# Optimization experiments

Hardware: AMD Instinct MI355X
Metric: run time of the kernel (lower is better)

Reference implementation:

```python
import jax, jax.numpy as jnp
import numpy as np

V, E, HID, T = 50000, 256, 512, 12   # vocab, embed dim, lstm hidden (bi total), tagset size
START, STOP = 10, 11
L = 2048                              # sentence length
H = HID // 2                          # per-direction hidden
NEG = -10000.0


def setup_inputs():
    key = jax.random.key(0)
    ks = jax.random.split(key, 13)
    s = 0.05
    sentence = jax.random.randint(ks[0], (L,), 0, V)
    embed = jax.random.normal(ks[1], (V, E), jnp.float32) * s
    w_ih_f = jax.random.normal(ks[2], (4 * H, E), jnp.float32) * s
    w_hh_f = jax.random.normal(ks[3], (4 * H, H), jnp.float32) * s
    b_ih_f = jax.random.normal(ks[4], (4 * H,), jnp.float32) * s
    b_hh_f = jax.random.normal(ks[5], (4 * H,), jnp.float32) * s
    w_ih_b = jax.random.normal(ks[6], (4 * H, E), jnp.float32) * s
    w_hh_b = jax.random.normal(ks[7], (4 * H, H), jnp.float32) * s
    b_ih_b = jax.random.normal(ks[8], (4 * H,), jnp.float32) * s
    b_hh_b = jax.random.normal(ks[9], (4 * H,), jnp.float32) * s
    w_out = jax.random.normal(ks[10], (T, HID), jnp.float32) * s
    b_out = jax.random.normal(ks[11], (T,), jnp.float32) * s
    transitions = jax.random.normal(ks[12], (T, T), jnp.float32)
    transitions = transitions.at[START, :].set(NEG).at[:, STOP].set(NEG)
    return dict(sentence=sentence, embed=embed,
                w_ih_f=w_ih_f, w_hh_f=w_hh_f, b_ih_f=b_ih_f, b_hh_f=b_hh_f,
                w_ih_b=w_ih_b, w_hh_b=w_hh_b, b_ih_b=b_ih_b, b_hh_b=b_hh_b,
                w_out=w_out, b_out=b_out, transitions=transitions)


def _lstm_dir(x, w_ih, w_hh, b, reverse):
    # x: [L, E] -> hs: [L, H]; PyTorch gate order i, f, g, o
    xg = x @ w_ih.T + b  # [L, 4H] precomputed input contribution

    def step(carry, xg_t):
        h, c = carry
        g = xg_t + h @ w_hh.T
        i, f, gg, o = jnp.split(g, 4)
        i, f, o = jax.nn.sigmoid(i), jax.nn.sigmoid(f), jax.nn.sigmoid(o)
        c = f * c + i * jnp.tanh(gg)
        h = o * jnp.tanh(c)
        return (h, c), h

    hdim = w_hh.shape[1]
    init = (jnp.zeros((hdim,), x.dtype), jnp.zeros((hdim,), x.dtype))
    _, hs = jax.lax.scan(step, init, xg, reverse=reverse)
    return hs


def _lstm_feats(sentence, embed, w_ih_f, w_hh_f, b_ih_f, b_hh_f,
                w_ih_b, w_hh_b, b_ih_b, b_hh_b, w_out, b_out):
    x = embed[sentence]                                        # [L, E]
    hf = _lstm_dir(x, w_ih_f, w_hh_f, b_ih_f + b_hh_f, False)  # [L, H]
    hb = _lstm_dir(x, w_ih_b, w_hh_b, b_ih_b + b_hh_b, True)   # [L, H]
    h = jnp.concatenate([hf, hb], axis=-1)                     # [L, 2H]
    return h @ w_out.T + b_out                                 # [L, T]


def reference(sentence, embed, w_ih_f, w_hh_f, b_ih_f, b_hh_f,
              w_ih_b, w_hh_b, b_ih_b, b_hh_b, w_out, b_out, transitions):
    feats = _lstm_feats(sentence, embed, w_ih_f, w_hh_f, b_ih_f, b_hh_f,
                        w_ih_b, w_hh_b, b_ih_b, b_hh_b, w_out, b_out)

    # Viterbi DP vectorized over tags, scanned over time
    init_v = jnp.full((T,), NEG, feats.dtype).at[START].set(0.0)

    def vstep(v, feat):
        scores = transitions + v[None, :]        # [next_tag, prev_tag]
        bp = jnp.argmax(scores, axis=1)          # best previous tag per next tag
        v_new = jnp.max(scores, axis=1) + feat
        return v_new, bp

    v, bps = jax.lax.scan(vstep, init_v, feats)  # bps: [L, T]
    terminal = v + transitions[STOP]
    best = jnp.argmax(terminal)
    path_score = terminal[best]

    def btrack(tag, bp):
        return bp[tag], tag

    _, best_path = jax.lax.scan(btrack, best, bps, reverse=True)  # [L] tags
    return path_score, best_path
```

## Files before the change

### kernel.cpp

```cpp
#include <hip/hip_runtime.h>

#define LSEQ 2048
#define TAGS 12

typedef _Float16 half2v __attribute__((ext_vector_type(2)));
typedef unsigned long long u64;

__device__ __forceinline__ float sigm(float x){ return 1.0f/(1.0f+__expf(-x)); }
__device__ __forceinline__ float tanh_fast(float x){ return 1.0f - 2.0f/(1.0f+__expf(2.0f*x)); }
__device__ __forceinline__ half2v pack2(float a, float b){
  half2v r; r.x=(_Float16)a; r.y=(_Float16)b; return r;
}

__global__ void init_kernel(u64* ex)
{
  int tid = blockIdx.x*256 + threadIdx.x;
  if (tid < 1024) ex[tid] = 0ull;
}

__global__ void xg_kernel(
    const int* sent, const float* embed,
    const float* w_ih_f, const float* b_ih_f, const float* b_hh_f,
    const float* w_ih_b, const float* b_ih_b, const float* b_hh_b,
    float* xg)
{
  __shared__ float x_sh[8][256];
  int tid = threadIdx.x;
  int t0 = blockIdx.x * 8;
  for (int i=0;i<8;++i){
    int idx = sent[t0+i];
    x_sh[i][tid] = embed[(size_t)idx*256 + tid];
  }
  __syncthreads();
  for (int ri=0; ri<8; ++ri){
    int r = ri*256 + tid;
    int d = r >> 10;
    int row = r & 1023;
    const float* wr = (d ? w_ih_b : w_ih_f) + (size_t)row*256;
    const float* bi = d ? b_ih_b : b_ih_f;
    const float* bh = d ? b_hh_b : b_hh_f;
    float acc[8];
    #pragma unroll
    for (int i=0;i<8;++i) acc[i]=0.f;
    for (int k0=0;k0<256;k0+=4){
      float4 p = *(const float4*)(wr + k0);
      #pragma unroll
      for (int i=0;i<8;++i){
        acc[i] += p.x*x_sh[i][k0] + p.y*x_sh[i][k0+1]
                + p.z*x_sh[i][k0+2] + p.w*x_sh[i][k0+3];
      }
    }
    float bias = bi[row] + bh[row];
    #pragma unroll
    for (int i=0;i<8;++i)
      xg[((size_t)d*LSEQ + (size_t)(t0+i))*1024 + row] = acc[i] + bias;
  }
}

__global__ __launch_bounds__(256,1) void lstm_rec(
    const float* __restrict__ w_hh_f, const float* __restrict__ w_hh_b,
    const float* __restrict__ xg, unsigned short* __restrict__ hstH,
    u64* __restrict__ ex)
{
  int blk = blockIdx.x;
  int d = blk & 7;
  if (d > 1) return;
  int q = blk >> 3;
  int qa = (q+1)&3, qb = (q+2)&3, qc = (q+3)&3;

  int tid = threadIdx.x;
  int g = tid >> 6, l = tid & 63;
  int row = g*256 + 64*q + l;
  const float* W = d ? w_hh_b : w_hh_f;
  const float* xgd = xg + (size_t)d*LSEQ*1024;
  unsigned short* hd = hstH + (size_t)d*LSEQ*256;
  u64* exd = ex + (size_t)d*256;

  __shared__ float gate_sh[256];
  __shared__ unsigned h2all[128];

  half2v w[128];
  {
    const float* p0 = W + (size_t)row*256 + 64*q;
    const float* p1 = W + (size_t)row*256 + 64*qa;
    const float* p2 = W + (size_t)row*256 + 64*qb;
    const float* p3 = W + (size_t)row*256 + 64*qc;
    #pragma unroll
    for (int k0=0;k0<16;++k0){
      float4 a = *(const float4*)(p0+4*k0);
      w[2*k0]      = pack2(a.x,a.y);  w[2*k0+1]    = pack2(a.z,a.w);
      float4 b = *(const float4*)(p1+4*k0);
      w[32+2*k0]   = pack2(b.x,b.y);  w[32+2*k0+1] = pack2(b.z,b.w);
      float4 cc= *(const float4*)(p2+4*k0);
      w[64+2*k0]   = pack2(cc.x,cc.y); w[64+2*k0+1] = pack2(cc.z,cc.w);
      float4 e = *(const float4*)(p3+4*k0);
      w[96+2*k0]   = pack2(e.x,e.y);  w[96+2*k0+1] = pack2(e.z,e.w);
    }
  }
  if (tid < 128) h2all[tid] = 0u;
  float c0 = 0.f, c1 = 0.f;
  unsigned hp = 0u;

  int pollj = tid - 64;
  int pollpeer = (q + 1 + (pollj>>5)) & 3;
  int pollslot = 32*pollpeer + (pollj & 31);
  int adrA = (l < 32) ? (32*qa + l) : (32*qb + (l-32));
  int adrB = 32*qc + (l & 31);
  int adrL = 32*q + (l & 31);
  __syncthreads();

  int tf = d ? (LSEQ-1) : 0;
  float xg0 = xgd[(size_t)tf*1024 + row];

  for (int s=0;s<LSEQ;++s){
    if (s > 0 && tid < 32){
      atomicExch(&exd[((s&1)<<7) + 32*q + tid], ((u64)(unsigned)s << 32) | (u64)hp);
      int tp = d ? (LSEQ-s) : (s-1);
      *(unsigned*)&hd[(size_t)tp*256 + 64*q + 2*tid] = hp;
    }
    u64 v0 = 0ull;
    bool poller = (s > 0) && (tid >= 64) && (tid < 160);
    if (poller)
      v0 = __hip_atomic_load(&exd[((s&1)<<7) + pollslot],
                             __ATOMIC_RELAXED, __HIP_MEMORY_SCOPE_AGENT);
    unsigned hl = h2all[adrL];
    float a0=xg0, a1=0.f, a2=0.f, a3=0.f;
    #pragma unroll
    for (int k=0;k<32;k+=4){
      unsigned p0v = __builtin_amdgcn_readlane(hl,k);
      unsigned p1v = __builtin_amdgcn_readlane(hl,k+1);
      unsigned p2v = __builtin_amdgcn_readlane(hl,k+2);
      unsigned p3v = __builtin_amdgcn_readlane(hl,k+3);
      a0 = __builtin_amdgcn_fdot2(__builtin_bit_cast(half2v,p0v), w[k],   a0, false);
      a1 = __builtin_amdgcn_fdot2(__builtin_bit_cast(half2v,p1v), w[k+1], a1, false);
      a2 = __builtin_amdgcn_fdot2(__builtin_bit_cast(half2v,p2v), w[k+2], a2, false);
      a3 = __builtin_amdgcn_fdot2(__builtin_bit_cast(half2v,p3v), w[k+3], a3, false);
    }
    if (poller){
      u64 v = v0;
      while ((unsigned)(v>>32) != (unsigned)s)
        v = __hip_atomic_load(&exd[((s&1)<<7) + pollslot],
                              __ATOMIC_RELAXED, __HIP_MEMORY_SCOPE_AGENT);
      h2all[pollslot] = (unsigned)v;
    }
    float nxg = 0.f;
    if (s+1 < LSEQ){
      int tn = d ? (LSEQ-2-s) : (s+1);
      nxg = xgd[(size_t)tn*1024 + row];
    }
    __syncthreads();
    unsigned hrA = h2all[adrA];
    unsigned hrB = h2all[adrB];
    #pragma unroll
    for (int k=0;k<32;k+=2){
      unsigned pA0 = __builtin_amdgcn_readlane(hrA, k);
      unsigned pA1 = __builtin_amdgcn_readlane(hrA, k+1);
      unsigned pB0 = __builtin_amdgcn_readlane(hrA, 32+k);
      unsigned pB1 = __builtin_amdgcn_readlane(hrA, 32+k+1);
      unsigned pC0 = __builtin_amdgcn_readlane(hrB, k);
      unsigned pC1 = __builtin_amdgcn_readlane(hrB, k+1);
      a0 = __builtin_amdgcn_fdot2(__builtin_bit_cast(half2v,pA0), w[32+k],   a0, false);
      a1 = __builtin_amdgcn_fdot2(__builtin_bit_cast(half2v,pA1), w[32+k+1], a1, false);
      a2 = __builtin_amdgcn_fdot2(__builtin_bit_cast(half2v,pB0), w[64+k],   a2, false);
      a3 = __builtin_amdgcn_fdot2(__builtin_bit_cast(half2v,pB1), w[64+k+1], a3, false);
      a0 = __builtin_amdgcn_fdot2(__builtin_bit_cast(half2v,pC0), w[96+k],   a0, false);
      a1 = __builtin_amdgcn_fdot2(__builtin_bit_cast(half2v,pC1), w[96+k+1], a1, false);
    }
    float pre = (a0+a1) + (a2+a3);
    float act = (g==2) ? tanh_fast(pre) : sigm(pre);
    gate_sh[tid] = act;
    xg0 = nxg;
    __syncthreads();
    if (tid < 32){
      int m = tid;
      float2 gi = *(const float2*)&gate_sh[      2*m];
      float2 gf = *(const float2*)&gate_sh[ 64 + 2*m];
      float2 gg = *(const float2*)&gate_sh[128 + 2*m];
      float2 go = *(const float2*)&gate_sh[192 + 2*m];
      c0 = gf.x*c0 + gi.x*gg.x;
      c1 = gf.y*c1 + gi.y*gg.y;
      float h0 = go.x * tanh_fast(c0);
      float h1 = go.y * tanh_fast(c1);
      hp = __builtin_bit_cast(unsigned, pack2(h0,h1));
      h2all[32*q + m] = hp;
    }
    __syncthreads();
  }
  if (tid < 32){
    int tl = d ? 0 : (LSEQ-1);
    *(unsigned*)&hd[(size_t)tl*256 + 64*q + 2*tid] = hp;
  }
}

__global__ void feats_kernel(
    const unsigned short* hstH, const float* w_out, const float* b_out,
    float* feats)
{
  __shared__ float w_sh[12*520];
  __shared__ float h_sh[16*520];
  const _Float16* hf = (const _Float16*)hstH;
  int tid=threadIdx.x;
  int t0=blockIdx.x*16;
  for (int i=tid;i<12*512;i+=256){ int tag=i>>9,k=i&511; w_sh[tag*520+k]=w_out[i]; }
  for (int i=tid;i<16*512;i+=256){
    int tt=i>>9,k=i&511;
    float v = (k<256)? (float)hf[(size_t)(t0+tt)*256+k]
                     : (float)hf[(size_t)(LSEQ+t0+tt)*256 + (k-256)];
    h_sh[tt*520+k]=v;
  }
  __syncthreads();
  if (tid<192){
    int tt=tid/12, tag=tid%12;
    const float* wr=&w_sh[tag*520];
    const float* hr=&h_sh[tt*520];
    float acc=b_out[tag];
    for (int k=0;k<512;k+=4){
      float4 a=*(const float4*)(wr+k);
      float4 b=*(const float4*)(hr+k);
      acc += a.x*b.x+a.y*b.y+a.z*b.z+a.w*b.w;
    }
    feats[(size_t)(t0+tt)*12+tag]=acc;
  }
}

__global__ void BiLSTM_CRF_14405320311361_kernel(
    const float* feats, const float* trans, float* outp)
{
  __shared__ float fsh[LSEQ*12];
  __shared__ unsigned char bps[LSEQ*12];
  __shared__ float term_sh[16];
  __shared__ int ibuf[66];
  __shared__ unsigned char fmap[64*12];
  int tid = threadIdx.x;
  for (int i=tid; i<LSEQ*12/4; i+=256)
    *(float4*)&fsh[4*i] = *(const float4*)&feats[4*i];
  __syncthreads();

  int lane = tid & 63;
  int fl = (lane<12) ? lane : 0;
  float vn = 0.f;
  if (tid < 64){
    float tr[12];
    #pragma unroll
    for (int p=0;p<12;++p) tr[p] = trans[fl*12+p];
    vn = (lane==10) ? 0.f : -10000.f;
    float fa = fsh[fl];
    float fb = fsh[12+fl];
    for (int t=0;t<LSEQ;++t){
      unsigned vu = __float_as_uint(vn);
      float best; int bp; float sc;
      best = tr[0] + __uint_as_float(__builtin_amdgcn_readlane(vu,0)); bp = 0;
      sc = tr[1]  + __uint_as_float(__builtin_amdgcn_readlane(vu,1));  if(sc>best){best=sc;bp=1;}
      sc = tr[2]  + __uint_as_float(__builtin_amdgcn_readlane(vu,2));  if(sc>best){best=sc;bp=2;}
      sc = tr[3]  + __uint_as_float(__builtin_amdgcn_readlane(vu,3));  if(sc>best){best=sc;bp=3;}
      sc = tr[4]  + __uint_as_float(__builtin_amdgcn_readlane(vu,4));  if(sc>best){best=sc;bp=4;}
      sc = tr[5]  + __uint_as_float(__builtin_amdgcn_readlane(vu,5));  if(sc>best){best=sc;bp=5;}
      sc = tr[6]  + __uint_as_float(__builtin_amdgcn_readlane(vu,6));  if(sc>best){best=sc;bp=6;}
      sc = tr[7]  + __uint_as_float(__builtin_amdgcn_readlane(vu,7));  if(sc>best){best=sc;bp=7;}
      sc = tr[8]  + __uint_as_float(__builtin_amdgcn_readlane(vu,8));  if(sc>best){best=sc;bp=8;}
      sc = tr[9]  + __uint_as_float(__builtin_amdgcn_readlane(vu,9));  if(sc>best){best=sc;bp=9;}
      sc = tr[10] + __uint_as_float(__builtin_amdgcn_readlane(vu,10)); if(sc>best){best=sc;bp=10;}
      sc = tr[11] + __uint_as_float(__builtin_amdgcn_readlane(vu,11)); if(sc>best){best=sc;bp=11;}
      vn = best + fa;
      fa = fb;
      if (t+2 < LSEQ) fb = fsh[(t+2)*12+fl];
      if (lane<12) bps[t*12+lane] = (unsigned char)bp;
    }
  }
  if (tid < 12) term_sh[tid] = vn + trans[11*12+tid];
  __syncthreads();
  if (tid == 0){
    float bs=term_sh[0]; int bt=0;
    for (int p=1;p<12;++p){ if (term_sh[p]>bs){bs=term_sh[p];bt=p;} }
    outp[0] = bs;
    ibuf[64] = bt;
  }
  __syncthreads();
  if (tid < 64){
    int b = tid;
    int f[12];
    int thi = b*32+31;
    #pragma unroll
    for (int x=0;x<12;++x) f[x] = bps[thi*12+x];
    for (int t=thi-1; t>=b*32; --t){
      int base = t*12;
      #pragma unroll
      for (int x=0;x<12;++x) f[x] = bps[base + f[x]];
    }
    #pragma unroll
    for (int x=0;x<12;++x) fmap[b*12+x] = (unsigned char)f[x];
  }
  __syncthreads();
  if (tid == 0){
    int tag = ibuf[64];
    for (int b=63;b>=0;--b){ ibuf[b]=tag; tag = fmap[b*12+tag]; }
  }
  __syncthreads();
  if (tid < 64){
    int b = tid;
    int tag = ibuf[b];
    for (int t=b*32+31; t>=b*32; --t){
      outp[1+t] = (float)tag;
      tag = bps[t*12+tag];
    }
  }
}

extern "C" void kernel_launch(void* const* d_in, const int* in_sizes, int n_in,
                              void* d_out, int out_size, void* d_ws, size_t ws_size,
                              hipStream_t stream) {
  const int*   sent   = (const int*)d_in[0];
  const float* embed  = (const float*)d_in[1];
  const float* w_ih_f = (const float*)d_in[2];
  const float* w_hh_f = (const float*)d_in[3];
  const float* b_ih_f = (const float*)d_in[4];
  const float* b_hh_f = (const float*)d_in[5];
  const float* w_ih_b = (const float*)d_in[6];
  const float* w_hh_b = (const float*)d_in[7];
  const float* b_ih_b = (const float*)d_in[8];
  const float* b_hh_b = (const float*)d_in[9];
  const float* w_out  = (const float*)d_in[10];
  const float* b_out  = (const float*)d_in[11];
  const float* trans  = (const float*)d_in[12];

  float* xg = (float*)d_ws;
  unsigned short* hstH = (unsigned short*)(xg + (size_t)2*LSEQ*1024);
  u64* ex = (u64*)(hstH + (size_t)2*LSEQ*256);
  float* feats = (float*)(ex + 1024);
  float* outp  = (float*)d_out;

  init_kernel<<<dim3(4), dim3(256), 0, stream>>>(ex);
  xg_kernel<<<dim3(LSEQ/8), dim3(256), 0, stream>>>(
      sent, embed, w_ih_f, b_ih_f, b_hh_f, w_ih_b, b_ih_b, b_hh_b, xg);
  lstm_rec<<<dim3(32), dim3(256), 0, stream>>>(w_hh_f, w_hh_b, xg, hstH, ex);
  feats_kernel<<<dim3(LSEQ/16), dim3(256), 0, stream>>>(hstH, w_out, b_out, feats);
  BiLSTM_CRF_14405320311361_kernel<<<dim3(1), dim3(256), 0, stream>>>(feats, trans, outp);
}
```

Before: 3.270 ms.

## Cut per-step barriers in LSTM recurrence via redundant cell update and double-buffered gates

Every thread now recomputes the LSTM cell update for its lane's hidden pair, so each wave already holds its local h in registers and reads it with readlane instead of through shared memory. The gate buffer is double-buffered, which drops the trailing barrier per timestep. The cross-block publish of h is moved to the end of the same step, right after h is computed. A lightweight custom barrier replaces __syncthreads. The aim is shorter per-step latency on the serial 2048-step critical path. The cost is redundant transcendental work in every wave and more delicate ordering between shared-memory accesses.

```diff
diff --git a/kernel.cpp b/kernel.cpp
--- a/kernel.cpp
+++ b/kernel.cpp
@@ -10,6 +10,13 @@
 __device__ __forceinline__ float tanh_fast(float x){ return 1.0f - 2.0f/(1.0f+__expf(2.0f*x)); }
 __device__ __forceinline__ half2v pack2(float a, float b){
   half2v r; r.x=(_Float16)a; r.y=(_Float16)b; return r;
+}
+
+__device__ __forceinline__ void wg_barrier(){
+  asm volatile("s_waitcnt lgkmcnt(0)" ::: "memory");
+  __builtin_amdgcn_s_barrier();
+  __builtin_amdgcn_sched_barrier(0);
+  asm volatile("" ::: "memory");
 }
 
 __global__ void init_kernel(u64* ex)
@@ -76,7 +83,7 @@
   unsigned short* hd = hstH + (size_t)d*LSEQ*256;
   u64* exd = ex + (size_t)d*256;
 
-  __shared__ float gate_sh[256];
+  __shared__ float gate_sh[2][256];
   __shared__ unsigned h2all[128];
 
   half2v w[128];
@@ -106,49 +113,44 @@
   int pollslot = 32*pollpeer + (pollj & 31);
   int adrA = (l < 32) ? (32*qa + l) : (32*qb + (l-32));
   int adrB = 32*qc + (l & 31);
-  int adrL = 32*q + (l & 31);
+  bool is_pub  = (tid < 32);
+  bool is_poll = (tid >= 64) && (tid < 160);
   __syncthreads();
 
   int tf = d ? (LSEQ-1) : 0;
   float xg0 = xgd[(size_t)tf*1024 + row];
 
   for (int s=0;s<LSEQ;++s){
-    if (s > 0 && tid < 32){
-      atomicExch(&exd[((s&1)<<7) + 32*q + tid], ((u64)(unsigned)s << 32) | (u64)hp);
-      int tp = d ? (LSEQ-s) : (s-1);
-      *(unsigned*)&hd[(size_t)tp*256 + 64*q + 2*tid] = hp;
-    }
     u64 v0 = 0ull;
-    bool poller = (s > 0) && (tid >= 64) && (tid < 160);
-    if (poller)
+    bool p = is_poll && (s > 0);
+    if (p)
       v0 = __hip_atomic_load(&exd[((s&1)<<7) + pollslot],
                              __ATOMIC_RELAXED, __HIP_MEMORY_SCOPE_AGENT);
-    unsigned hl = h2all[adrL];
     float a0=xg0, a1=0.f, a2=0.f, a3=0.f;
     #pragma unroll
     for (int k=0;k<32;k+=4){
-      unsigned p0v = __builtin_amdgcn_readlane(hl,k);
-      unsigned p1v = __builtin_amdgcn_readlane(hl,k+1);
-      unsigned p2v = __builtin_amdgcn_readlane(hl,k+2);
-      unsigned p3v = __builtin_amdgcn_readlane(hl,k+3);
+      unsigned p0v = __builtin_amdgcn_readlane(hp,k);
+      unsigned p1v = __builtin_amdgcn_readlane(hp,k+1);
+      unsigned p2v = __builtin_amdgcn_readlane(hp,k+2);
+      unsigned p3v = __builtin_amdgcn_readlane(hp,k+3);
       a0 = __builtin_amdgcn_fdot2(__builtin_bit_cast(half2v,p0v), w[k],   a0, false);
       a1 = __builtin_amdgcn_fdot2(__builtin_bit_cast(half2v,p1v), w[k+1], a1, false);
       a2 = __builtin_amdgcn_fdot2(__builtin_bit_cast(half2v,p2v), w[k+2], a2, false);
       a3 = __builtin_amdgcn_fdot2(__builtin_bit_cast(half2v,p3v), w[k+3], a3, false);
     }
-    if (poller){
+    float nxg = 0.f;
+    if (s+1 < LSEQ){
+      int tn = d ? (LSEQ-2-s) : (s+1);
+      nxg = xgd[(size_t)tn*1024 + row];
+    }
+    if (p){
       u64 v = v0;
       while ((unsigned)(v>>32) != (unsigned)s)
         v = __hip_atomic_load(&exd[((s&1)<<7) + pollslot],
                               __ATOMIC_RELAXED, __HIP_MEMORY_SCOPE_AGENT);
       h2all[pollslot] = (unsigned)v;
     }
-    float nxg = 0.f;
-    if (s+1 < LSEQ){
-      int tn = d ? (LSEQ-2-s) : (s+1);
-      nxg = xgd[(size_t)tn*1024 + row];
-    }
-    __syncthreads();
+    wg_barrier();
     unsigned hrA = h2all[adrA];
     unsigned hrB = h2all[adrB];
     #pragma unroll
@@ -168,27 +170,29 @@
     }
     float pre = (a0+a1) + (a2+a3);
     float act = (g==2) ? tanh_fast(pre) : sigm(pre);
-    gate_sh[tid] = act;
-    xg0 = nxg;
-    __syncthreads();
-    if (tid < 32){
-      int m = tid;
-      float2 gi = *(const float2*)&gate_sh[      2*m];
-      float2 gf = *(const float2*)&gate_sh[ 64 + 2*m];
-      float2 gg = *(const float2*)&gate_sh[128 + 2*m];
-      float2 go = *(const float2*)&gate_sh[192 + 2*m];
+    gate_sh[s&1][tid] = act;
+    wg_barrier();
+    {
+      int m = l & 31;
+      const float* gp = gate_sh[s&1];
+      float2 gi = *(const float2*)&gp[      2*m];
+      float2 gf = *(const float2*)&gp[ 64 + 2*m];
+      float2 gg = *(const float2*)&gp[128 + 2*m];
+      float2 go = *(const float2*)&gp[192 + 2*m];
       c0 = gf.x*c0 + gi.x*gg.x;
       c1 = gf.y*c1 + gi.y*gg.y;
       float h0 = go.x * tanh_fast(c0);
       float h1 = go.y * tanh_fast(c1);
       hp = __builtin_bit_cast(unsigned, pack2(h0,h1));
-      h2all[32*q + m] = hp;
-    }
-    __syncthreads();
-  }
-  if (tid < 32){
-    int tl = d ? 0 : (LSEQ-1);
-    *(unsigned*)&hd[(size_t)tl*256 + 64*q + 2*tid] = hp;
+    }
+    if (is_pub){
+      if (s+1 < LSEQ)
+        atomicExch(&exd[(((s+1)&1)<<7) + 32*q + tid],
+                   ((u64)(unsigned)(s+1) << 32) | (u64)hp);
+      int tp = d ? (LSEQ-1-s) : s;
+      *(unsigned*)&hd[(size_t)tp*256 + 64*q + 2*tid] = hp;
+    }
+    xg0 = nxg;
   }
 }
 
```

Result: slower. 3.577 ms (+9.4%).
